# Optimization experiments

Measured on AMD Instinct MI355X. Metric: run time of the kernel, lower is better.

## Reference

```python
import jax, jax.numpy as jnp
import numpy as np

N_NODES = 100000
N_EDGES = 3200000
D_IN = 256
D_HID = 256
D_OUT = 64


def setup_inputs() -> dict:
    key = jax.random.key(0)
    k1, k2, k3, k4 = jax.random.split(key, 4)
    x = jax.random.normal(k1, (N_NODES, D_IN), dtype=jnp.float32)
    edge_index = jax.random.randint(k2, (2, N_EDGES), 0, N_NODES, dtype=jnp.int32)
    W1 = jax.random.normal(k3, (D_IN, D_HID), dtype=jnp.float32) / np.sqrt(D_IN)
    b1 = jnp.zeros((D_HID,), dtype=jnp.float32)
    W2 = jax.random.normal(k4, (D_HID, D_OUT), dtype=jnp.float32) / np.sqrt(D_HID)
    b2 = jnp.zeros((D_OUT,), dtype=jnp.float32)
    return {"x": x, "edge_index": edge_index, "W1": W1, "b1": b1, "W2": W2, "b2": b2}


def _gcn_conv(x, src, dst, norm, W, b, n_nodes):
    # dense linear transform, then normalized scatter-add aggregation
    h = x @ W  # [N, out]
    msg = norm[:, None] * h[src]  # gather + scale, [E+N, out]
    out = jax.ops.segment_sum(msg, dst, num_segments=n_nodes)
    return out + b


def reference(x, edge_index, W1, b1, W2, b2):
    n = x.shape[0]
    # add self-loops (PyG GCNConv default)
    loops = jnp.arange(n, dtype=edge_index.dtype)
    src = jnp.concatenate([edge_index[0], loops])
    dst = jnp.concatenate([edge_index[1], loops])
    # symmetric normalization deg^{-1/2}[src] * deg^{-1/2}[dst]
    deg = jax.ops.segment_sum(jnp.ones_like(src, dtype=x.dtype), dst, num_segments=n)
    dinv = jnp.where(deg > 0, jax.lax.rsqrt(jnp.maximum(deg, 1.0)), 0.0)
    norm = dinv[src] * dinv[dst]

    h = _gcn_conv(x, src, dst, norm, W1, b1, n)
    h = jax.nn.relu(h)
    # dropout is identity at inference
    h = _gcn_conv(h, src, dst, norm, W2, b2, n)
    return jax.nn.log_softmax(h, axis=1)
```

## Files before the change

kernel.cpp:

```cpp
#include <hip/hip_runtime.h>
#include <hip/hip_bf16.h>


typedef __bf16 bf16;
typedef bf16 bf16x4 __attribute__((ext_vector_type(4)));
typedef bf16 bf16x8 __attribute__((ext_vector_type(8)));
typedef float f32x4 __attribute__((ext_vector_type(4)));
typedef signed char s8;
typedef s8 s8x8 __attribute__((ext_vector_type(8)));

#define NBLK 256

__global__ __launch_bounds__(256) void k_b1(const int* __restrict__ edge, int E, int chunk,
                                            int NB, int* __restrict__ gcnt) {
    __shared__ int cnt[512];
    int tid = threadIdx.x;
    for (int i = tid; i < NB; i += 256) cnt[i] = 0;
    __syncthreads();
    int s = blockIdx.x * chunk, e = min(s + chunk, E);
    for (int i = s + tid; i < e; i += 256) atomicAdd(&cnt[edge[E + i] >> 9], 1);
    __syncthreads();
    for (int i = tid; i < NB; i += 256) gcnt[blockIdx.x * NB + i] = cnt[i];
}

__global__ void k_b2(const int* __restrict__ gcnt, int NB, int E, int* __restrict__ bstart) {
    __shared__ int col[256];
    int k = threadIdx.x;
    int sum = 0;
    if (k < NB)
        for (int b = 0; b < NBLK; ++b) sum += gcnt[b * NB + k];
    col[k] = sum;
    __syncthreads();
    for (int o = 1; o < 256; o <<= 1) {
        int v = (k >= o) ? col[k - o] : 0;
        __syncthreads();
        col[k] += v;
        __syncthreads();
    }
    if (k < NB) bstart[k] = col[k] - sum;
    if (k == 0) bstart[NB] = E;
}

__global__ void k_b2b(int* __restrict__ gcnt, int NB, const int* __restrict__ bstart) {
    __shared__ int col[256];
    int b = threadIdx.x;
    int k = blockIdx.x;
    int v = gcnt[b * NB + k];
    col[b] = v;
    __syncthreads();
    for (int o = 1; o < 256; o <<= 1) {
        int t = (b >= o) ? col[b - o] : 0;
        __syncthreads();
        col[b] += t;
        __syncthreads();
    }
    gcnt[b * NB + k] = bstart[k] + col[b] - v;
}

__global__ __launch_bounds__(256) void k_b3(const int* __restrict__ edge, int E, int chunk,
                                            int NB, const int* __restrict__ base,
                                            int* __restrict__ ebuf) {
    __shared__ int cnt[512];
    __shared__ int bs[512];
    int tid = threadIdx.x;
    for (int i = tid; i < NB; i += 256) {
        cnt[i] = 0;
        bs[i] = base[blockIdx.x * NB + i];
    }
    __syncthreads();
    int s = blockIdx.x * chunk, e = min(s + chunk, E);
    for (int i = s + tid; i < e; i += 256) {
        int sv = edge[i], dv = edge[E + i];
        int k = dv >> 9;
        int r = atomicAdd(&cnt[k], 1);
        ebuf[bs[k] + r] = sv | ((dv & 511) << 17);
    }
}

__global__ __launch_bounds__(256) void k_b45(const int* __restrict__ ebuf,
                                             const int* __restrict__ bstart, int n, int E,
                                             int NB, int* __restrict__ off,
                                             float* __restrict__ dinv) {
    __shared__ int cnt[512];
    __shared__ int red[256];
    int tid = threadIdx.x;
    int k = blockIdx.x;
    cnt[tid] = 0;
    cnt[tid + 256] = 0;
    __syncthreads();
    int s = bstart[k], e = bstart[k + 1];
    for (int i = s + tid; i < e; i += 256) atomicAdd(&cnt[(ebuf[i] >> 17) & 511], 1);
    __syncthreads();
    int c0 = cnt[tid * 2], c1 = cnt[tid * 2 + 1];
    int sum = c0 + c1;
    red[tid] = sum;
    __syncthreads();
    for (int o = 1; o < 256; o <<= 1) {
        int v = (tid >= o) ? red[tid - o] : 0;
        __syncthreads();
        red[tid] += v;
        __syncthreads();
    }
    int ex = red[tid] - sum;
    int base = k << 9;
    int g0 = base + tid * 2, g1 = g0 + 1;
    int o0 = s + ex, o1 = s + ex + c0;
    if (g0 < n) { off[g0] = o0; dinv[g0] = rsqrtf((float)(c0 + 1)); }
    else if (g0 == n) off[g0] = o0;
    if (g1 < n) { off[g1] = o1; dinv[g1] = rsqrtf((float)(c1 + 1)); }
    else if (g1 == n) off[g1] = o1;
    if (k == NB - 1 && tid == 0) off[n] = E;
}

__global__ __launch_bounds__(256) void k_b6(const int* __restrict__ ebuf,
                                            const int* __restrict__ bstart,
                                            const int* __restrict__ off,
                                            const float* __restrict__ dinv,
                                            const float* __restrict__ scale, int n,
                                            int2* __restrict__ pair) {
    __shared__ int cnt[512];
    __shared__ int offl[512];
    int tid = threadIdx.x;
    int k = blockIdx.x;
    int base = k << 9;
    cnt[tid] = 0;
    cnt[tid + 256] = 0;
    offl[tid] = (base + tid < n) ? off[base + tid] : 0;
    offl[tid + 256] = (base + 256 + tid < n) ? off[base + 256 + tid] : 0;
    __syncthreads();
    int s = bstart[k], e = bstart[k + 1];
    for (int i = s + tid; i < e; i += 256) {
        int pk = ebuf[i];
        int sv = pk & 0x1ffff;
        int node = (pk >> 17) & 511;
        int r = atomicAdd(&cnt[node], 1);
        float w = dinv[sv] * scale[sv];
        pair[offl[node] + r] = make_int2(sv, __float_as_int(w));
    }
}

__global__ __launch_bounds__(256) void k_quant(const float* __restrict__ x,
                                               unsigned char* __restrict__ xq,
                                               float* __restrict__ scale, int n) {
    int row = blockIdx.x * 4 + (threadIdx.x >> 6);
    int lane = threadIdx.x & 63;
    if (row >= n) return;
    f32x4 v = ((const f32x4*)x)[(size_t)row * 64 + lane];
    float m = fmaxf(fmaxf(fabsf(v[0]), fabsf(v[1])), fmaxf(fabsf(v[2]), fabsf(v[3])));
    for (int o = 32; o > 0; o >>= 1) m = fmaxf(m, __shfl_xor(m, o));
    m = fmaxf(m, 1e-20f);
    float inv = 127.0f / m;
    int b0 = (__float2int_rn(v[0] * inv) + 128) & 255;
    int b1 = (__float2int_rn(v[1] * inv) + 128) & 255;
    int b2 = (__float2int_rn(v[2] * inv) + 128) & 255;
    int b3 = (__float2int_rn(v[3] * inv) + 128) & 255;
    ((int*)xq)[(size_t)row * 64 + lane] = b0 | (b1 << 8) | (b2 << 16) | (b3 << 24);
    if (lane == 0) scale[row] = m / 127.0f;
}

__global__ __launch_bounds__(256) void k_quant2(const bf16* __restrict__ tb,
                                                const float* __restrict__ scale,
                                                s8* __restrict__ tq,
                                                float* __restrict__ tscale,
                                                float* __restrict__ r2, int n) {
    int t = blockIdx.x * 256 + threadIdx.x;
    int row = t >> 3;
    int l8 = t & 7;
    if (row >= n) return;
    bf16x8 v = ((const bf16x8*)tb)[(size_t)row * 8 + l8];
    float f[8], m = 0.0f;
#pragma unroll
    for (int j = 0; j < 8; ++j) { f[j] = (float)v[j]; m = fmaxf(m, fabsf(f[j])); }
    for (int o = 4; o > 0; o >>= 1) m = fmaxf(m, __shfl_xor(m, o));
    m = fmaxf(m, 1e-20f);
    float inv = 127.0f / m;
    int lo = 0, hi = 0;
#pragma unroll
    for (int j = 0; j < 4; ++j) lo |= (__float2int_rn(f[j] * inv) & 255) << (8 * j);
#pragma unroll
    for (int j = 0; j < 4; ++j) hi |= (__float2int_rn(f[4 + j] * inv) & 255) << (8 * j);
    ((int2*)tq)[(size_t)row * 8 + l8] = make_int2(lo, hi);
    if (l8 == 0) {
        float s = m / 127.0f;
        tscale[row] = s;
        r2[row] = s / scale[row];
    }
}

__global__ void k_wt(const float* __restrict__ W, bf16* __restrict__ Wt, int NC) {
    int nc = blockIdx.x;
    int k = threadIdx.x;
    Wt[nc * 256 + k] = (bf16)W[k * NC + nc];
}

__device__ __forceinline__ void acc16(float a[16], uint4 t, float w, float& wsum) {
    wsum += w;
    unsigned u0 = t.x, u1 = t.y, u2 = t.z, u3 = t.w;
    a[0]  += w * (float)(u0 & 255u);
    a[1]  += w * (float)((u0 >> 8) & 255u);
    a[2]  += w * (float)((u0 >> 16) & 255u);
    a[3]  += w * (float)(u0 >> 24);
    a[4]  += w * (float)(u1 & 255u);
    a[5]  += w * (float)((u1 >> 8) & 255u);
    a[6]  += w * (float)((u1 >> 16) & 255u);
    a[7]  += w * (float)(u1 >> 24);
    a[8]  += w * (float)(u2 & 255u);
    a[9]  += w * (float)((u2 >> 8) & 255u);
    a[10] += w * (float)((u2 >> 16) & 255u);
    a[11] += w * (float)(u2 >> 24);
    a[12] += w * (float)(u3 & 255u);
    a[13] += w * (float)((u3 >> 8) & 255u);
    a[14] += w * (float)((u3 >> 16) & 255u);
    a[15] += w * (float)(u3 >> 24);
}

__global__ __launch_bounds__(256) void k_agg1(const unsigned char* __restrict__ xq,
                                              const float* __restrict__ scale,
                                              const int* __restrict__ off,
                                              const int2* __restrict__ pair,
                                              const float* __restrict__ dinv,
                                              bf16* __restrict__ ax, int n) {
    int wv = blockIdx.x * 4 + (threadIdx.x >> 6);
    int lane = threadIdx.x & 63;
    int node = wv * 4 + (lane >> 4);
    int l16 = lane & 15;
    if (node >= n) return;
    int s0 = off[node], s1 = off[node + 1];
    float dv = dinv[node];
    float a[16] = {};
    float wsum = 0.0f;
    uint4 xs = *(const uint4*)(xq + (size_t)node * 256 + l16 * 16);
    acc16(a, xs, dv * scale[node], wsum);
    int e = s0;
    for (; e + 4 <= s1; e += 4) {
        int2 p[4];
#pragma unroll
        for (int q = 0; q < 4; ++q) p[q] = pair[e + q];
        uint4 t[4];
#pragma unroll
        for (int q = 0; q < 4; ++q)
            t[q] = *(const uint4*)(xq + (size_t)p[q].x * 256 + l16 * 16);
#pragma unroll
        for (int q = 0; q < 4; ++q) acc16(a, t[q], __int_as_float(p[q].y), wsum);
    }
    for (; e < s1; ++e) {
        int2 p = pair[e];
        uint4 t = *(const uint4*)(xq + (size_t)p.x * 256 + l16 * 16);
        acc16(a, t, __int_as_float(p.y), wsum);
    }
    float c = 128.0f * wsum;
    bf16x8 o0, o1;
#pragma unroll
    for (int j = 0; j < 8; ++j) o0[j] = (bf16)((a[j] - c) * dv);
#pragma unroll
    for (int j = 0; j < 8; ++j) o1[j] = (bf16)((a[8 + j] - c) * dv);
    ((bf16x8*)ax)[(size_t)node * 32 + l16 * 2] = o0;
    ((bf16x8*)ax)[(size_t)node * 32 + l16 * 2 + 1] = o1;
}

__global__ __launch_bounds__(256) void k_gemmp(const bf16* __restrict__ A,
                                               const bf16* __restrict__ Bt,
                                               const float* __restrict__ bias,
                                               bf16* __restrict__ C, int n) {
    __shared__ __align__(16) bf16 As[4 * 64 * 8];
    __shared__ __align__(16) bf16 Bs[16 * 64 * 8];
    int tid = threadIdx.x;
    int bm = blockIdx.x * 64;
    int w = tid >> 6, lane = tid & 63;

    int r = tid >> 2;
    int cq = tid & 3;
    int a_idx = (((r >> 4) * 64) + cq * 16 + (r & 15)) * 8;
    int arow = bm + r; if (arow > n - 1) arow = n - 1;

    f32x4 acc[16] = {};

    for (int k0 = 0; k0 < 256; k0 += 32) {
        __syncthreads();
        uint4 av = *(const uint4*)(A + (size_t)arow * 256 + k0 + cq * 8);
        *(uint4*)(As + a_idx) = av;
#pragma unroll
        for (int rep = 0; rep < 4; ++rep) {
            int r2 = rep * 64 + r;
            uint4 bv = *(const uint4*)(Bt + (size_t)r2 * 256 + k0 + cq * 8);
            *(uint4*)(Bs + (((r2 >> 4) * 64) + cq * 16 + (r2 & 15)) * 8) = bv;
        }
        __syncthreads();
        bf16x8 af = *(const bf16x8*)(As + (w * 64 + lane) * 8);
#pragma unroll
        for (int ct = 0; ct < 16; ++ct) {
            bf16x8 bfr = *(const bf16x8*)(Bs + (ct * 64 + lane) * 8);
            acc[ct] = __builtin_amdgcn_mfma_f32_16x16x32_bf16(af, bfr, acc[ct], 0, 0, 0);
        }
    }

    int colb = lane & 15, rowq = lane >> 4;
#pragma unroll
    for (int ct = 0; ct < 16; ++ct) {
        int col = ct * 16 + colb;
        float bv = bias[col];
#pragma unroll
        for (int rr = 0; rr < 4; ++rr) {
            int row = bm + w * 16 + rowq * 4 + rr;
            if (row < n) {
                float v = acc[ct][rr] + bv;
                C[(size_t)row * 256 + col] = (bf16)(v > 0.0f ? v : 0.0f);
            }
        }
    }
}

__global__ __launch_bounds__(256) void k_gemm2(const bf16* __restrict__ A,
                                               const bf16* __restrict__ Bt,
                                               bf16* __restrict__ C, int n) {
    __shared__ __align__(16) bf16 As[4 * 64 * 8];
    __shared__ __align__(16) bf16 Bs[4 * 64 * 8];
    int tid = threadIdx.x;
    int bm = blockIdx.x * 64;
    int w = tid >> 6, lane = tid & 63;
    int wm = w >> 1, wn = w & 1;

    int r = tid >> 2;
    int cq = tid & 3;
    int lds_idx = (((r >> 4) * 64) + cq * 16 + (r & 15)) * 8;
    int arow = bm + r; if (arow > n - 1) arow = n - 1;

    f32x4 acc[2][2] = {};

    for (int k0 = 0; k0 < 256; k0 += 32) {
        __syncthreads();
        uint4 av = *(const uint4*)(A + (size_t)arow * 256 + k0 + cq * 8);
        uint4 bv = *(const uint4*)(Bt + (size_t)r * 256 + k0 + cq * 8);
        *(uint4*)(As + lds_idx) = av;
        *(uint4*)(Bs + lds_idx) = bv;
        __syncthreads();
#pragma unroll
        for (int i = 0; i < 2; ++i) {
            bf16x8 af = *(const bf16x8*)(As + ((wm * 2 + i) * 64 + lane) * 8);
#pragma unroll
            for (int j = 0; j < 2; ++j) {
                bf16x8 bfr = *(const bf16x8*)(Bs + ((wn * 2 + j) * 64 + lane) * 8);
                acc[i][j] = __builtin_amdgcn_mfma_f32_16x16x32_bf16(af, bfr, acc[i][j], 0, 0, 0);
            }
        }
    }

    int colb = lane & 15, rowq = lane >> 4;
#pragma unroll
    for (int i = 0; i < 2; ++i) {
#pragma unroll
        for (int j = 0; j < 2; ++j) {
            int col = wn * 32 + j * 16 + colb;
#pragma unroll
            for (int rr = 0; rr < 4; ++rr) {
                int row = bm + wm * 32 + i * 16 + rowq * 4 + rr;
                if (row < n) C[(size_t)row * 64 + col] = (bf16)acc[i][j][rr];
            }
        }
    }
}

__global__ __launch_bounds__(256) void k_agg2(const s8* __restrict__ tq,
                                              const float* __restrict__ tscale,
                                              const float* __restrict__ r2,
                                              const int* __restrict__ off,
                                              const int2* __restrict__ pair,
                                              const float* __restrict__ dinv,
                                              const float* __restrict__ b2,
                                              float* __restrict__ out, int n) {
    int wv = blockIdx.x * 4 + (threadIdx.x >> 6);
    int lane = threadIdx.x & 63;
    int node = wv * 8 + (lane >> 3);
    int l8 = lane & 7;
    if (node >= n) return;
    int s0 = off[node], s1 = off[node + 1];
    float dv = dinv[node];
    const s8x8* T = (const s8x8*)tq;
    s8x8 ts = T[(size_t)node * 8 + l8];
    float ws = dv * tscale[node];
    float a[8];
#pragma unroll
    for (int j = 0; j < 8; ++j) a[j] = ws * (float)ts[j];
    int e = s0;
    for (; e + 4 <= s1; e += 4) {
        int2 p[4];
#pragma unroll
        for (int q = 0; q < 4; ++q) p[q] = pair[e + q];
        float sc[4];
#pragma unroll
        for (int q = 0; q < 4; ++q) sc[q] = r2[p[q].x];
        s8x8 tv[4];
#pragma unroll
        for (int q = 0; q < 4; ++q) tv[q] = T[(size_t)p[q].x * 8 + l8];
#pragma unroll
        for (int q = 0; q < 4; ++q) {
            float w = __int_as_float(p[q].y) * sc[q];
#pragma unroll
            for (int j = 0; j < 8; ++j) a[j] += w * (float)tv[q][j];
        }
    }
    for (; e < s1; ++e) {
        int2 p = pair[e];
        float w = __int_as_float(p.y) * r2[p.x];
        s8x8 tv = T[(size_t)p.x * 8 + l8];
#pragma unroll
        for (int j = 0; j < 8; ++j) a[j] += w * (float)tv[j];
    }
    const float4* B2 = (const float4*)b2;
    float4 bv0 = B2[l8 * 2], bv1 = B2[l8 * 2 + 1];
    a[0] = a[0] * dv + bv0.x; a[1] = a[1] * dv + bv0.y;
    a[2] = a[2] * dv + bv0.z; a[3] = a[3] * dv + bv0.w;
    a[4] = a[4] * dv + bv1.x; a[5] = a[5] * dv + bv1.y;
    a[6] = a[6] * dv + bv1.z; a[7] = a[7] * dv + bv1.w;
    float m = a[0];
#pragma unroll
    for (int j = 1; j < 8; ++j) m = fmaxf(m, a[j]);
    for (int o = 4; o > 0; o >>= 1) m = fmaxf(m, __shfl_xor(m, o));
    float s = 0.0f;
#pragma unroll
    for (int j = 0; j < 8; ++j) s += __expf(a[j] - m);
    for (int o = 4; o > 0; o >>= 1) s += __shfl_xor(s, o);
    float ls = m + __logf(s);
    f32x4 o0, o1;
    o0[0] = a[0] - ls; o0[1] = a[1] - ls; o0[2] = a[2] - ls; o0[3] = a[3] - ls;
    o1[0] = a[4] - ls; o1[1] = a[5] - ls; o1[2] = a[6] - ls; o1[3] = a[7] - ls;
    f32x4* O = (f32x4*)out;
    O[(size_t)node * 16 + l8 * 2] = o0;
    O[(size_t)node * 16 + l8 * 2 + 1] = o1;
}

extern "C" void kernel_launch(void* const* d_in, const int* in_sizes, int n_in,
                              void* d_out, int out_size, void* d_ws, size_t ws_size,
                              hipStream_t stream) {
    const float* x   = (const float*)d_in[0];
    const int*  edge = (const int*)d_in[1];
    const float* W1  = (const float*)d_in[2];
    const float* b1  = (const float*)d_in[3];
    const float* W2  = (const float*)d_in[4];
    const float* b2  = (const float*)d_in[5];
    float* out = (float*)d_out;

    int n = in_sizes[0] / 256;
    int E = in_sizes[1] / 2;
    int NB = (n + 511) >> 9;
    int chunk = (E + NBLK - 1) / NBLK;

    char* ws = (char*)d_ws;
    auto alloc = [&](size_t bytes) -> char* {
        char* p = ws;
        ws += (bytes + 255) & ~(size_t)255;
        return p;
    };
    int*   gcnt   = (int*)alloc((size_t)NBLK * NB * 4);
    int*   bstart = (int*)alloc((size_t)(NB + 1) * 4);
    int*   ebuf   = (int*)alloc((size_t)E * 4);
    float* dinv   = (float*)alloc((size_t)n * 4);
    int*   off    = (int*)alloc((size_t)(n + 1) * 4);
    int2*  pair   = (int2*)alloc((size_t)E * 8);
    unsigned char* xq = (unsigned char*)alloc((size_t)n * 256);
    float* scale  = (float*)alloc((size_t)n * 4);
    bf16*  ax     = (bf16*)alloc((size_t)n * 256 * 2);
    bf16*  h1     = (bf16*)alloc((size_t)n * 256 * 2);
    bf16*  tb     = (bf16*)alloc((size_t)n * 64 * 2);
    s8*    tq     = (s8*)alloc((size_t)n * 64);
    float* tscale = (float*)alloc((size_t)n * 4);
    float* r2     = (float*)alloc((size_t)n * 4);
    bf16*  W1t    = (bf16*)alloc(256 * 256 * 2);
    bf16*  W2t    = (bf16*)alloc(64 * 256 * 2);

    k_quant<<<(n + 3) / 4, 256, 0, stream>>>(x, xq, scale, n);

    k_b1<<<NBLK, 256, 0, stream>>>(edge, E, chunk, NB, gcnt);
    k_b2<<<1, 256, 0, stream>>>(gcnt, NB, E, bstart);
    k_b2b<<<NB, 256, 0, stream>>>(gcnt, NB, bstart);
    k_b3<<<NBLK, 256, 0, stream>>>(edge, E, chunk, NB, gcnt, ebuf);
    k_b45<<<NB, 256, 0, stream>>>(ebuf, bstart, n, E, NB, off, dinv);
    k_b6<<<NB, 256, 0, stream>>>(ebuf, bstart, off, dinv, scale, n, pair);

    k_wt<<<256, 256, 0, stream>>>(W1, W1t, 256);
    k_wt<<<64, 256, 0, stream>>>(W2, W2t, 64);

    k_agg1<<<(n + 15) / 16, 256, 0, stream>>>(xq, scale, off, pair, dinv, ax, n);
    k_gemmp<<<(n + 63) / 64, 256, 0, stream>>>(ax, W1t, b1, h1, n);

    k_gemm2<<<(n + 63) / 64, 256, 0, stream>>>(h1, W2t, tb, n);
    k_quant2<<<(n * 8 + 255) / 256, 256, 0, stream>>>(tb, scale, tq, tscale, r2, n);
    k_agg2<<<(n + 31) / 32, 256, 0, stream>>>(tq, tscale, r2, off, pair, dinv, b2, out, n);
}
```

Measured before the change: 562.5 us.

## Prefetch edge pairs in aggregation, swizzle GEMM LDS, precompute per-node edge weights

The aggregation loops in both layers now software-pipeline the edge-pair loads, fetching the next four pairs (and r2 scales in layer 2) while the current gathered rows are accumulated, so more memory requests are in flight. Layer-2 quantization switches to offset-128 unsigned bytes with a weight-sum correction, letting it reuse the same unpack-and-accumulate path as layer 1. Both GEMM kernels apply an XOR swizzle to LDS slots to reduce bank conflicts. The per-source weight dinv*scale is computed once per node in k_b45 instead of per edge in k_b6, removing one random gather per edge at the cost of an extra n-sized buffer.

Result: faster. 543.8 us (-3.3%).

```diff
diff --git a/kernel.cpp b/kernel.cpp
--- a/kernel.cpp
+++ b/kernel.cpp
@@ -7,7 +7,6 @@
 typedef bf16 bf16x8 __attribute__((ext_vector_type(8)));
 typedef float f32x4 __attribute__((ext_vector_type(4)));
 typedef signed char s8;
-typedef s8 s8x8 __attribute__((ext_vector_type(8)));
 
 #define NBLK 256
 
@@ -78,9 +77,11 @@
 }
 
 __global__ __launch_bounds__(256) void k_b45(const int* __restrict__ ebuf,
-                                             const int* __restrict__ bstart, int n, int E,
+                                             const int* __restrict__ bstart,
+                                             const float* __restrict__ scale, int n, int E,
                                              int NB, int* __restrict__ off,
-                                             float* __restrict__ dinv) {
+                                             float* __restrict__ dinv,
+                                             float* __restrict__ ws) {
     __shared__ int cnt[512];
     __shared__ int red[256];
     int tid = threadIdx.x;
@@ -105,18 +106,25 @@
     int base = k << 9;
     int g0 = base + tid * 2, g1 = g0 + 1;
     int o0 = s + ex, o1 = s + ex + c0;
-    if (g0 < n) { off[g0] = o0; dinv[g0] = rsqrtf((float)(c0 + 1)); }
-    else if (g0 == n) off[g0] = o0;
-    if (g1 < n) { off[g1] = o1; dinv[g1] = rsqrtf((float)(c1 + 1)); }
-    else if (g1 == n) off[g1] = o1;
+    if (g0 < n) {
+        off[g0] = o0;
+        float d0 = rsqrtf((float)(c0 + 1));
+        dinv[g0] = d0;
+        ws[g0] = d0 * scale[g0];
+    } else if (g0 == n) off[g0] = o0;
+    if (g1 < n) {
+        off[g1] = o1;
+        float d1 = rsqrtf((float)(c1 + 1));
+        dinv[g1] = d1;
+        ws[g1] = d1 * scale[g1];
+    } else if (g1 == n) off[g1] = o1;
     if (k == NB - 1 && tid == 0) off[n] = E;
 }
 
 __global__ __launch_bounds__(256) void k_b6(const int* __restrict__ ebuf,
                                             const int* __restrict__ bstart,
                                             const int* __restrict__ off,
-                                            const float* __restrict__ dinv,
-                                            const float* __restrict__ scale, int n,
+                                            const float* __restrict__ ws, int n,
                                             int2* __restrict__ pair) {
     __shared__ int cnt[512];
     __shared__ int offl[512];
@@ -134,8 +142,7 @@
         int sv = pk & 0x1ffff;
         int node = (pk >> 17) & 511;
         int r = atomicAdd(&cnt[node], 1);
-        float w = dinv[sv] * scale[sv];
-        pair[offl[node] + r] = make_int2(sv, __float_as_int(w));
+        pair[offl[node] + r] = make_int2(sv, __float_as_int(ws[sv]));
     }
 }
 
@@ -160,7 +167,7 @@
 
 __global__ __launch_bounds__(256) void k_quant2(const bf16* __restrict__ tb,
                                                 const float* __restrict__ scale,
-                                                s8* __restrict__ tq,
+                                                unsigned char* __restrict__ tq,
                                                 float* __restrict__ tscale,
                                                 float* __restrict__ r2, int n) {
     int t = blockIdx.x * 256 + threadIdx.x;
@@ -176,9 +183,9 @@
     float inv = 127.0f / m;
     int lo = 0, hi = 0;
 #pragma unroll
-    for (int j = 0; j < 4; ++j) lo |= (__float2int_rn(f[j] * inv) & 255) << (8 * j);
-#pragma unroll
-    for (int j = 0; j < 4; ++j) hi |= (__float2int_rn(f[4 + j] * inv) & 255) << (8 * j);
+    for (int j = 0; j < 4; ++j) lo |= ((__float2int_rn(f[j] * inv) + 128) & 255) << (8 * j);
+#pragma unroll
+    for (int j = 0; j < 4; ++j) hi |= ((__float2int_rn(f[4 + j] * inv) + 128) & 255) << (8 * j);
     ((int2*)tq)[(size_t)row * 8 + l8] = make_int2(lo, hi);
     if (l8 == 0) {
         float s = m / 127.0f;
@@ -214,6 +221,19 @@
     a[15] += w * (float)(u3 >> 24);
 }
 
+__device__ __forceinline__ void acc8(float a[8], int2 t, float w, float& wsum) {
+    wsum += w;
+    unsigned u0 = (unsigned)t.x, u1 = (unsigned)t.y;
+    a[0] += w * (float)(u0 & 255u);
+    a[1] += w * (float)((u0 >> 8) & 255u);
+    a[2] += w * (float)((u0 >> 16) & 255u);
+    a[3] += w * (float)(u0 >> 24);
+    a[4] += w * (float)(u1 & 255u);
+    a[5] += w * (float)((u1 >> 8) & 255u);
+    a[6] += w * (float)((u1 >> 16) & 255u);
+    a[7] += w * (float)(u1 >> 24);
+}
+
 __global__ __launch_bounds__(256) void k_agg1(const unsigned char* __restrict__ xq,
                                               const float* __restrict__ scale,
                                               const int* __restrict__ off,
@@ -232,10 +252,24 @@
     uint4 xs = *(const uint4*)(xq + (size_t)node * 256 + l16 * 16);
     acc16(a, xs, dv * scale[node], wsum);
     int e = s0;
-    for (; e + 4 <= s1; e += 4) {
+    if (s1 - s0 >= 4) {
         int2 p[4];
 #pragma unroll
-        for (int q = 0; q < 4; ++q) p[q] = pair[e + q];
+        for (int q = 0; q < 4; ++q) p[q] = pair[s0 + q];
+        e = s0 + 4;
+        for (; e + 4 <= s1; e += 4) {
+            uint4 t[4];
+#pragma unroll
+            for (int q = 0; q < 4; ++q)
+                t[q] = *(const uint4*)(xq + (size_t)p[q].x * 256 + l16 * 16);
+            int2 pn[4];
+#pragma unroll
+            for (int q = 0; q < 4; ++q) pn[q] = pair[e + q];
+#pragma unroll
+            for (int q = 0; q < 4; ++q) acc16(a, t[q], __int_as_float(p[q].y), wsum);
+#pragma unroll
+            for (int q = 0; q < 4; ++q) p[q] = pn[q];
+        }
         uint4 t[4];
 #pragma unroll
         for (int q = 0; q < 4; ++q)
@@ -257,6 +291,8 @@
     ((bf16x8*)ax)[(size_t)node * 32 + l16 * 2] = o0;
     ((bf16x8*)ax)[(size_t)node * 32 + l16 * 2 + 1] = o1;
 }
+
+__device__ __forceinline__ int swz(int s) { return s ^ ((s >> 3) & 7); }
 
 __global__ __launch_bounds__(256) void k_gemmp(const bf16* __restrict__ A,
                                                const bf16* __restrict__ Bt,
@@ -270,7 +306,7 @@
 
     int r = tid >> 2;
     int cq = tid & 3;
-    int a_idx = (((r >> 4) * 64) + cq * 16 + (r & 15)) * 8;
+    int a_slot = swz(((r >> 4) * 64) + cq * 16 + (r & 15));
     int arow = bm + r; if (arow > n - 1) arow = n - 1;
 
     f32x4 acc[16] = {};
@@ -278,18 +314,18 @@
     for (int k0 = 0; k0 < 256; k0 += 32) {
         __syncthreads();
         uint4 av = *(const uint4*)(A + (size_t)arow * 256 + k0 + cq * 8);
-        *(uint4*)(As + a_idx) = av;
+        *(uint4*)(As + a_slot * 8) = av;
 #pragma unroll
         for (int rep = 0; rep < 4; ++rep) {
             int r2 = rep * 64 + r;
             uint4 bv = *(const uint4*)(Bt + (size_t)r2 * 256 + k0 + cq * 8);
-            *(uint4*)(Bs + (((r2 >> 4) * 64) + cq * 16 + (r2 & 15)) * 8) = bv;
-        }
-        __syncthreads();
-        bf16x8 af = *(const bf16x8*)(As + (w * 64 + lane) * 8);
+            *(uint4*)(Bs + swz(((r2 >> 4) * 64) + cq * 16 + (r2 & 15)) * 8) = bv;
+        }
+        __syncthreads();
+        bf16x8 af = *(const bf16x8*)(As + swz(w * 64 + lane) * 8);
 #pragma unroll
         for (int ct = 0; ct < 16; ++ct) {
-            bf16x8 bfr = *(const bf16x8*)(Bs + (ct * 64 + lane) * 8);
+            bf16x8 bfr = *(const bf16x8*)(Bs + swz(ct * 64 + lane) * 8);
             acc[ct] = __builtin_amdgcn_mfma_f32_16x16x32_bf16(af, bfr, acc[ct], 0, 0, 0);
         }
     }
@@ -322,7 +358,7 @@
 
     int r = tid >> 2;
     int cq = tid & 3;
-    int lds_idx = (((r >> 4) * 64) + cq * 16 + (r & 15)) * 8;
+    int lds_slot = swz(((r >> 4) * 64) + cq * 16 + (r & 15));
     int arow = bm + r; if (arow > n - 1) arow = n - 1;
 
     f32x4 acc[2][2] = {};
@@ -331,15 +367,15 @@
         __syncthreads();
         uint4 av = *(const uint4*)(A + (size_t)arow * 256 + k0 + cq * 8);
         uint4 bv = *(const uint4*)(Bt + (size_t)r * 256 + k0 + cq * 8);
-        *(uint4*)(As + lds_idx) = av;
-        *(uint4*)(Bs + lds_idx) = bv;
+        *(uint4*)(As + lds_slot * 8) = av;
+        *(uint4*)(Bs + lds_slot * 8) = bv;
         __syncthreads();
 #pragma unroll
         for (int i = 0; i < 2; ++i) {
-            bf16x8 af = *(const bf16x8*)(As + ((wm * 2 + i) * 64 + lane) * 8);
+            bf16x8 af = *(const bf16x8*)(As + swz((wm * 2 + i) * 64 + lane) * 8);
 #pragma unroll
             for (int j = 0; j < 2; ++j) {
-                bf16x8 bfr = *(const bf16x8*)(Bs + ((wn * 2 + j) * 64 + lane) * 8);
+                bf16x8 bfr = *(const bf16x8*)(Bs + swz((wn * 2 + j) * 64 + lane) * 8);
                 acc[i][j] = __builtin_amdgcn_mfma_f32_16x16x32_bf16(af, bfr, acc[i][j], 0, 0, 0);
             }
         }
@@ -360,7 +396,7 @@
     }
 }
 
-__global__ __launch_bounds__(256) void k_agg2(const s8* __restrict__ tq,
+__global__ __launch_bounds__(256) void k_agg2(const unsigned char* __restrict__ tq,
                                               const float* __restrict__ tscale,
                                               const float* __restrict__ r2,
                                               const int* __restrict__ off,
@@ -375,43 +411,53 @@
     if (node >= n) return;
     int s0 = off[node], s1 = off[node + 1];
     float dv = dinv[node];
-    const s8x8* T = (const s8x8*)tq;
-    s8x8 ts = T[(size_t)node * 8 + l8];
-    float ws = dv * tscale[node];
-    float a[8];
-#pragma unroll
-    for (int j = 0; j < 8; ++j) a[j] = ws * (float)ts[j];
+    const int2* T = (const int2*)tq;
+    int2 ts = T[(size_t)node * 8 + l8];
+    float a[8] = {};
+    float wsum = 0.0f;
+    acc8(a, ts, dv * tscale[node], wsum);
     int e = s0;
-    for (; e + 4 <= s1; e += 4) {
-        int2 p[4];
-#pragma unroll
-        for (int q = 0; q < 4; ++q) p[q] = pair[e + q];
-        float sc[4];
+    if (s1 - s0 >= 4) {
+        int2 p[4]; float sc[4];
+#pragma unroll
+        for (int q = 0; q < 4; ++q) p[q] = pair[s0 + q];
 #pragma unroll
         for (int q = 0; q < 4; ++q) sc[q] = r2[p[q].x];
-        s8x8 tv[4];
-#pragma unroll
-        for (int q = 0; q < 4; ++q) tv[q] = T[(size_t)p[q].x * 8 + l8];
-#pragma unroll
-        for (int q = 0; q < 4; ++q) {
-            float w = __int_as_float(p[q].y) * sc[q];
-#pragma unroll
-            for (int j = 0; j < 8; ++j) a[j] += w * (float)tv[q][j];
-        }
+        e = s0 + 4;
+        for (; e + 4 <= s1; e += 4) {
+            int2 t[4];
+#pragma unroll
+            for (int q = 0; q < 4; ++q) t[q] = T[(size_t)p[q].x * 8 + l8];
+            int2 pn[4];
+#pragma unroll
+            for (int q = 0; q < 4; ++q) pn[q] = pair[e + q];
+            float scn[4];
+#pragma unroll
+            for (int q = 0; q < 4; ++q) scn[q] = r2[pn[q].x];
+#pragma unroll
+            for (int q = 0; q < 4; ++q) acc8(a, t[q], __int_as_float(p[q].y) * sc[q], wsum);
+#pragma unroll
+            for (int q = 0; q < 4; ++q) { p[q] = pn[q]; sc[q] = scn[q]; }
+        }
+        int2 t[4];
+#pragma unroll
+        for (int q = 0; q < 4; ++q) t[q] = T[(size_t)p[q].x * 8 + l8];
+#pragma unroll
+        for (int q = 0; q < 4; ++q) acc8(a, t[q], __int_as_float(p[q].y) * sc[q], wsum);
     }
     for (; e < s1; ++e) {
         int2 p = pair[e];
         float w = __int_as_float(p.y) * r2[p.x];
-        s8x8 tv = T[(size_t)p.x * 8 + l8];
-#pragma unroll
-        for (int j = 0; j < 8; ++j) a[j] += w * (float)tv[j];
-    }
+        int2 t = T[(size_t)p.x * 8 + l8];
+        acc8(a, t, w, wsum);
+    }
+    float c = 128.0f * wsum;
     const float4* B2 = (const float4*)b2;
     float4 bv0 = B2[l8 * 2], bv1 = B2[l8 * 2 + 1];
-    a[0] = a[0] * dv + bv0.x; a[1] = a[1] * dv + bv0.y;
-    a[2] = a[2] * dv + bv0.z; a[3] = a[3] * dv + bv0.w;
-    a[4] = a[4] * dv + bv1.x; a[5] = a[5] * dv + bv1.y;
-    a[6] = a[6] * dv + bv1.z; a[7] = a[7] * dv + bv1.w;
+    a[0] = (a[0] - c) * dv + bv0.x; a[1] = (a[1] - c) * dv + bv0.y;
+    a[2] = (a[2] - c) * dv + bv0.z; a[3] = (a[3] - c) * dv + bv0.w;
+    a[4] = (a[4] - c) * dv + bv1.x; a[5] = (a[5] - c) * dv + bv1.y;
+    a[6] = (a[6] - c) * dv + bv1.z; a[7] = (a[7] - c) * dv + bv1.w;
     float m = a[0];
 #pragma unroll
     for (int j = 1; j < 8; ++j) m = fmaxf(m, a[j]);
@@ -455,6 +501,7 @@
     int*   bstart = (int*)alloc((size_t)(NB + 1) * 4);
     int*   ebuf   = (int*)alloc((size_t)E * 4);
     float* dinv   = (float*)alloc((size_t)n * 4);
+    float* wsv    = (float*)alloc((size_t)n * 4);
     int*   off    = (int*)alloc((size_t)(n + 1) * 4);
     int2*  pair   = (int2*)alloc((size_t)E * 8);
     unsigned char* xq = (unsigned char*)alloc((size_t)n * 256);
@@ -462,7 +509,7 @@
     bf16*  ax     = (bf16*)alloc((size_t)n * 256 * 2);
     bf16*  h1     = (bf16*)alloc((size_t)n * 256 * 2);
     bf16*  tb     = (bf16*)alloc((size_t)n * 64 * 2);
-    s8*    tq     = (s8*)alloc((size_t)n * 64);
+    unsigned char* tq = (unsigned char*)alloc((size_t)n * 64);
     float* tscale = (float*)alloc((size_t)n * 4);
     float* r2     = (float*)alloc((size_t)n * 4);
     bf16*  W1t    = (bf16*)alloc(256 * 256 * 2);
@@ -474,8 +521,8 @@
     k_b2<<<1, 256, 0, stream>>>(gcnt, NB, E, bstart);
     k_b2b<<<NB, 256, 0, stream>>>(gcnt, NB, bstart);
     k_b3<<<NBLK, 256, 0, stream>>>(edge, E, chunk, NB, gcnt, ebuf);
-    k_b45<<<NB, 256, 0, stream>>>(ebuf, bstart, n, E, NB, off, dinv);
-    k_b6<<<NB, 256, 0, stream>>>(ebuf, bstart, off, dinv, scale, n, pair);
+    k_b45<<<NB, 256, 0, stream>>>(ebuf, bstart, scale, n, E, NB, off, dinv, wsv);
+    k_b6<<<NB, 256, 0, stream>>>(ebuf, bstart, off, wsv, n, pair);
 
     k_wt<<<256, 256, 0, stream>>>(W1, W1t, 256);
     k_wt<<<64, 256, 0, stream>>>(W2, W2t, 64);
```
